# Performance work log

Hardware: AMD Instinct MI355X
Metric: run time of the kernel (lower is better)

## Reference

```python
import jax, jax.numpy as jnp
import numpy as np

B, T_ENC, T_DEC = 16, 256, 64
N_MEL = 80
ENC_DIM = 512
ATTN_RNN_DIM = 1024
DEC_RNN_DIM = 1024
PRENET_DIM = 256
ATTN_DIM = 128
LOC_FILTERS = 32
LOC_KERNEL = 31


def setup_inputs() -> dict:
    key = jax.random.key(0)
    ks = jax.random.split(key, 32)
    s = 0.02
    inp = {
        "memory": jax.random.normal(ks[0], (B, T_ENC, ENC_DIM), jnp.float32),
        "decoder_inputs": jax.random.normal(ks[1], (B, N_MEL, T_DEC), jnp.float32),
        "memory_lengths": jax.random.randint(ks[2], (B,), T_ENC // 2, T_ENC + 1, jnp.int32),
        # prenet
        "prenet_W1": jax.random.normal(ks[3], (PRENET_DIM, N_MEL), jnp.float32) * s,
        "prenet_b1": jnp.zeros((PRENET_DIM,), jnp.float32),
        "prenet_W2": jax.random.normal(ks[4], (PRENET_DIM, PRENET_DIM), jnp.float32) * s,
        "prenet_b2": jnp.zeros((PRENET_DIM,), jnp.float32),
        # attention LSTMCell: input = prenet_dim + enc_dim
        "attn_rnn_Wih": jax.random.normal(ks[5], (4 * ATTN_RNN_DIM, PRENET_DIM + ENC_DIM), jnp.float32) * s,
        "attn_rnn_Whh": jax.random.normal(ks[6], (4 * ATTN_RNN_DIM, ATTN_RNN_DIM), jnp.float32) * s,
        "attn_rnn_bih": jnp.zeros((4 * ATTN_RNN_DIM,), jnp.float32),
        "attn_rnn_bhh": jnp.zeros((4 * ATTN_RNN_DIM,), jnp.float32),
        # attention projections (bias-free, Tacotron2 style)
        "query_W": jax.random.normal(ks[7], (ATTN_DIM, ATTN_RNN_DIM), jnp.float32) * s,
        "mem_W": jax.random.normal(ks[8], (ATTN_DIM, ENC_DIM), jnp.float32) * s,
        "loc_conv_W": jax.random.normal(ks[9], (LOC_FILTERS, 2, LOC_KERNEL), jnp.float32) * s,
        "loc_dense_W": jax.random.normal(ks[10], (ATTN_DIM, LOC_FILTERS), jnp.float32) * s,
        "attn_v": jax.random.normal(ks[11], (1, ATTN_DIM), jnp.float32) * s,
        # decoder LSTMCell: input = attn_rnn_dim + enc_dim
        "dec_rnn_Wih": jax.random.normal(ks[12], (4 * DEC_RNN_DIM, ATTN_RNN_DIM + ENC_DIM), jnp.float32) * s,
        "dec_rnn_Whh": jax.random.normal(ks[13], (4 * DEC_RNN_DIM, DEC_RNN_DIM), jnp.float32) * s,
        "dec_rnn_bih": jnp.zeros((4 * DEC_RNN_DIM,), jnp.float32),
        "dec_rnn_bhh": jnp.zeros((4 * DEC_RNN_DIM,), jnp.float32),
        # output heads
        "proj_W": jax.random.normal(ks[14], (N_MEL, DEC_RNN_DIM + ENC_DIM), jnp.float32) * s,
        "proj_b": jnp.zeros((N_MEL,), jnp.float32),
        "gate_W": jax.random.normal(ks[15], (1, DEC_RNN_DIM + ENC_DIM), jnp.float32) * s,
        "gate_b": jnp.zeros((1,), jnp.float32),
    }
    return inp


def _lstm_cell(x, h, c, Wih, Whh, bih, bhh):
    gates = x @ Wih.T + bih + h @ Whh.T + bhh  # [B, 4H]
    i, f, g, o = jnp.split(gates, 4, axis=-1)
    c2 = jax.nn.sigmoid(f) * c + jax.nn.sigmoid(i) * jnp.tanh(g)
    h2 = jax.nn.sigmoid(o) * jnp.tanh(c2)
    return h2, c2


def _decoder_forward(memory, decoder_inputs, memory_lengths,
                     prenet_W1, prenet_b1, prenet_W2, prenet_b2,
                     attn_rnn_Wih, attn_rnn_Whh, attn_rnn_bih, attn_rnn_bhh,
                     query_W, mem_W, loc_conv_W, loc_dense_W, attn_v,
                     dec_rnn_Wih, dec_rnn_Whh, dec_rnn_bih, dec_rnn_bhh,
                     proj_W, proj_b, gate_W, gate_b):
    b, t_enc, _ = memory.shape
    t_dec = decoder_inputs.shape[2]
    # parse_decoder_inputs: [B,80,T] -> [T,B,80]; prepend go frame
    frames = jnp.transpose(decoder_inputs, (2, 0, 1))  # [T,B,80]
    go = jnp.zeros((1, b, N_MEL), frames.dtype)
    frames = jnp.concatenate([go, frames], axis=0)  # [T+1,B,80]
    # prenet (dropout disabled for determinism)
    pre = jax.nn.relu(frames @ prenet_W1.T + prenet_b1)
    pre = jax.nn.relu(pre @ prenet_W2.T + prenet_b2)  # [T+1,B,256]
    pre = pre[:-1]  # steps use frames 0..T-1

    processed_memory = memory @ mem_W.T  # [B,T_enc,128]
    pad_mask = jnp.arange(t_enc)[None, :] >= memory_lengths[:, None]  # [B,T_enc] True=pad

    pad = (LOC_KERNEL - 1) // 2

    def step(carry, x_t):
        (ah, ac, dh, dc, aw, aw_cum, ctx) = carry
        cell_in = jnp.concatenate([x_t, ctx], axis=-1)
        ah, ac = _lstm_cell(cell_in, ah, ac, attn_rnn_Wih, attn_rnn_Whh, attn_rnn_bih, attn_rnn_bhh)
        # location-sensitive attention
        awc = jnp.stack([aw, aw_cum], axis=1)  # [B,2,T_enc]
        loc = jax.lax.conv_general_dilated(
            awc, loc_conv_W, window_strides=(1,), padding=[(pad, pad)],
            dimension_numbers=("NCH", "OIH", "NCH"))  # [B,32,T_enc]
        loc = jnp.transpose(loc, (0, 2, 1)) @ loc_dense_W.T  # [B,T_enc,128]
        query = (ah @ query_W.T)[:, None, :]  # [B,1,128]
        energies = jnp.squeeze(jnp.tanh(query + processed_memory + loc) @ attn_v.T, -1)  # [B,T_enc]
        energies = jnp.where(pad_mask, -1e9, energies)
        aw = jax.nn.softmax(energies, axis=1)
        ctx = jnp.einsum("bt,btd->bd", aw, memory)
        aw_cum = aw_cum + aw
        dec_in = jnp.concatenate([ah, ctx], axis=-1)
        dh, dc = _lstm_cell(dec_in, dh, dc, dec_rnn_Wih, dec_rnn_Whh, dec_rnn_bih, dec_rnn_bhh)
        dhc = jnp.concatenate([dh, ctx], axis=-1)
        mel = dhc @ proj_W.T + proj_b  # [B,80]
        gate = jnp.squeeze(dhc @ gate_W.T + gate_b, -1)  # [B]
        return (ah, ac, dh, dc, aw, aw_cum, ctx), (mel, gate, aw)

    z = jnp.zeros
    carry0 = (z((b, ATTN_RNN_DIM)), z((b, ATTN_RNN_DIM)),
              z((b, DEC_RNN_DIM)), z((b, DEC_RNN_DIM)),
              z((b, t_enc)), z((b, t_enc)), z((b, ENC_DIM)))
    _, (mels, gates, aligns) = jax.lax.scan(step, carry0, pre)
    # parse_decoder_outputs
    mel_outputs = jnp.transpose(mels, (1, 2, 0))  # [B,80,T_dec]
    gate_outputs = jnp.transpose(gates, (1, 0))  # [B,T_dec]
    alignments = jnp.transpose(aligns, (1, 0, 2))  # [B,T_dec,T_enc]
    return mel_outputs, gate_outputs, alignments


def reference(memory, decoder_inputs, memory_lengths,
              prenet_W1, prenet_b1, prenet_W2, prenet_b2,
              attn_rnn_Wih, attn_rnn_Whh, attn_rnn_bih, attn_rnn_bhh,
              query_W, mem_W, loc_conv_W, loc_dense_W, attn_v,
              dec_rnn_Wih, dec_rnn_Whh, dec_rnn_bih, dec_rnn_bhh,
              proj_W, proj_b, gate_W, gate_b):
    return _decoder_forward(memory, decoder_inputs, memory_lengths,
                            prenet_W1, prenet_b1, prenet_W2, prenet_b2,
                            attn_rnn_Wih, attn_rnn_Whh, attn_rnn_bih, attn_rnn_bhh,
                            query_W, mem_W, loc_conv_W, loc_dense_W, attn_v,
                            dec_rnn_Wih, dec_rnn_Whh, dec_rnn_bih, dec_rnn_bhh,
                            proj_W, proj_b, gate_W, gate_b)
```

## Files before the change

kernel.cpp:

```cpp
#include <hip/hip_runtime.h>

typedef __attribute__((ext_vector_type(8))) short short8;
typedef __attribute__((ext_vector_type(4))) float f32x4;
typedef unsigned short u16;
typedef unsigned int u32;
typedef unsigned long long u64;


static constexpr size_t OFF_WFA   = 0;
static constexpr size_t OFF_WFD   = 14680064;
static constexpr size_t OFF_PREF  = 35651584;
static constexpr size_t OFF_QWF   = 36175872;
static constexpr size_t OFF_MWT   = 36438016;
static constexpr size_t OFF_BA    = 36700160;
static constexpr size_t OFF_BD    = 36716544;
static constexpr size_t OFF_PM    = 36732928;
static constexpr size_t OFF_CTXF  = 38830080;
static constexpr size_t OFF_DHF   = 40960000;
static constexpr size_t OFF_AHFD  = 45219840;
static constexpr size_t OFF_CTXFD = 47349760;
static constexpr size_t OFF_DHFD  = 48414720;
static constexpr size_t OFF_BAR   = 50544640;
static constexpr size_t OFF_END   = 50548736;

__device__ __forceinline__ float sigmf(float x) { return 1.f / (1.f + expf(-x)); }
__device__ __forceinline__ float tanh_fast(float x) {
  float e2 = __expf(2.f * x);
  return 1.f - 2.f / (e2 + 1.f);
}
__device__ __forceinline__ u16 f2bf(float f) {
  u32 u = __float_as_uint(f);
  return (u16)((u + 0x7FFFu + ((u >> 16) & 1u)) >> 16);
}
__device__ __forceinline__ float bf2f(u16 x) { return __uint_as_float(((u32)x) << 16); }

__device__ __forceinline__ short8 ld_frag_nt(const void* p) {
  const u64* q = (const u64*)p;
  u64 lo = __builtin_nontemporal_load(q);
  u64 hi = __builtin_nontemporal_load(q + 1);
  union { u64 q2[2]; short8 s; } u;
  u.q2[0] = lo; u.q2[1] = hi;
  return u.s;
}

__device__ __forceinline__ void st_u16_agent(u16* p, u16 v) {
  __hip_atomic_store(p, v, __ATOMIC_RELAXED, __HIP_MEMORY_SCOPE_AGENT);
}
__device__ __forceinline__ void st_f32_agent(float* p, float v) {
  __hip_atomic_store(p, v, __ATOMIC_RELAXED, __HIP_MEMORY_SCOPE_AGENT);
}
__device__ __forceinline__ void st_u64_agent(u64* p, u64 v) {
  __hip_atomic_store(p, v, __ATOMIC_RELAXED, __HIP_MEMORY_SCOPE_AGENT);
}
__device__ __forceinline__ u32 ld_u32_agent(const u32* p) {
  return __hip_atomic_load(p, __ATOMIC_RELAXED, __HIP_MEMORY_SCOPE_AGENT);
}
__device__ __forceinline__ void st_u32_agent(u32* p, u32 v) {
  __hip_atomic_store(p, v, __ATOMIC_RELAXED, __HIP_MEMORY_SCOPE_AGENT);
}

template <int SLP>
__device__ __forceinline__ void wait_one(const u32* f, u32 target, int th) {
  if (th == 0) {
    while (ld_u32_agent(f) < target) __builtin_amdgcn_s_sleep(SLP);
  }
  __syncthreads();
}

__global__ void k_wfrag(const float* __restrict__ Wih, const float* __restrict__ Whh,
                        char* __restrict__ dst, int NT, int Kih) {
  int idx = blockIdx.x * 256 + threadIdx.x;
  int l = idx & 63;
  int st = idx >> 6;
  int s = st % NT, tile = st / NT;
  int r = l & 15, kg = l >> 4;
  int j = (r >> 2) * 1024 + tile * 4 + (r & 3);
  int k0 = s * 32 + kg * 8;
  const float* src = (k0 < Kih) ? (Wih + (size_t)j * Kih + k0)
                                : (Whh + (size_t)j * 1024 + (k0 - Kih));
  short8 v;
#pragma unroll
  for (int e = 0; e < 8; ++e) v[e] = (short)f2bf(src[e]);
  *(short8*)(dst + (size_t)idx * 16) = v;
}

__global__ void k_qwfrag(const float* __restrict__ qW, char* __restrict__ dst) {
  int idx = blockIdx.x * 256 + threadIdx.x;
  int l = idx & 63, tile = idx >> 6;
  int dt = tile >> 5, kt = tile & 31;
  int j = dt * 16 + (l & 15);
  int k0 = kt * 32 + (l >> 4) * 8;
  short8 v;
#pragma unroll
  for (int e = 0; e < 8; ++e) v[e] = (short)f2bf(qW[j * 1024 + k0 + e]);
  *(short8*)(dst + (size_t)idx * 16) = v;
}

__global__ void k_smallprep(const float* __restrict__ memW,
                            const float* __restrict__ abih, const float* __restrict__ abhh,
                            const float* __restrict__ dbih, const float* __restrict__ dbhh,
                            char* __restrict__ wsb) {
  int idx = blockIdx.x * 256 + threadIdx.x;
  if (idx < 65536) {
    int k = idx >> 7, d = idx & 127;
    ((float*)(wsb + OFF_MWT))[idx] = memW[d * 512 + k];
  } else if (idx < 69632) {
    int j = idx - 65536;
    ((float*)(wsb + OFF_BA))[j] = abih[j] + abhh[j];
  } else if (idx < 73728) {
    int j = idx - 69632;
    ((float*)(wsb + OFF_BD))[j] = dbih[j] + dbhh[j];
  }
}

__global__ void k_prenet(const float* __restrict__ dec_in,
                         const float* __restrict__ W1, const float* __restrict__ b1,
                         const float* __restrict__ W2, const float* __restrict__ b2,
                         char* __restrict__ wsb) {
  int s = blockIdx.x, b = blockIdx.y, th = threadIdx.x;
  __shared__ float frame[80];
  __shared__ float h1[256];
  if (th < 80) frame[th] = (s == 0) ? 0.f : dec_in[(b * 80 + th) * 64 + (s - 1)];
  __syncthreads();
  float a = b1[th];
  const float* w1r = W1 + th * 80;
  for (int m = 0; m < 80; ++m) a += w1r[m] * frame[m];
  h1[th] = fmaxf(a, 0.f);
  __syncthreads();
  float a2 = b2[th];
  const float* w2r = W2 + th * 256;
  for (int i = 0; i < 256; ++i) a2 += w2r[i] * h1[i];
  float pre = fmaxf(a2, 0.f);
  int k = th;
  ((u16*)(wsb + OFF_PREF))[(((size_t)s * 8 + (k >> 5)) * 64 + ((k >> 3) & 3) * 16 + b) * 8 + (k & 7)] = f2bf(pre);
}

__global__ void k_pm(const float* __restrict__ memory, char* __restrict__ wsb) {
  int bk = blockIdx.x, th = threadIdx.x;
  int b = bk >> 4, t0 = (bk & 15) * 16;
  __shared__ float mrow[16 * 512];
  for (int i = 0; i < 8; ++i) {
    int fi4 = i * 256 + th;
    int tl = fi4 >> 7, k4 = (fi4 & 127) << 2;
    *(float4*)&mrow[tl * 512 + k4] =
        *(const float4*)&memory[((size_t)(b * 256 + t0 + tl)) * 512 + k4];
  }
  __syncthreads();
  int d = th & 127, tl0 = th >> 7;
  float acc[8] = {};
  const float* mWT = (const float*)(wsb + OFF_MWT);
  float* pmw = (float*)(wsb + OFF_PM);
  for (int k = 0; k < 512; ++k) {
    float w = mWT[k * 128 + d];
#pragma unroll
    for (int i = 0; i < 8; ++i) acc[i] += w * mrow[(tl0 + i * 2) * 512 + k];
  }
  for (int i = 0; i < 8; ++i)
    pmw[((size_t)(b * 256 + t0 + tl0 + i * 2)) * 128 + d] = acc[i];
}

struct KParams {
  const float* memory;
  const int* mlen;
  const float* convW;
  const float* ldW;
  const float* attnv;
  const float* projW;
  const float* projb;
  const float* gateW;
  const float* gateb;
  char* wsb;
  float* out;
};

__device__ __forceinline__ f32x4 attn_early(char* wsb, int t, int kc, int l,
                                            const short8* afE) {
  f32x4 acc = {0.f, 0.f, 0.f, 0.f};
#pragma unroll
  for (int i = 0; i < 10; ++i) {
    int pe = kc * 10 + i;
    const char* src = (pe < 8)
        ? wsb + OFF_PREF + (((size_t)t * 8 + pe) * 64 + l) * 16
        : wsb + OFF_AHFD + (((size_t)t * 32 + (pe - 8)) * 64 + l) * 16;
    short8 bv = ld_frag_nt(src);
    acc = __builtin_amdgcn_mfma_f32_16x16x32_bf16(afE[i], bv, acc, 0, 0, 0);
  }
  return acc;
}

__device__ __forceinline__ void run_dec(char* wsb, int t, int tb, int th, int l, int w,
                                        int rt, int kc, float biasD_r, float& cD,
                                        float* smC) {
  const char* wfd = wsb + OFF_WFD;
  int tIdx = tb * 2 + rt;
  f32x4 acc = {0.f, 0.f, 0.f, 0.f};
#pragma unroll
  for (int i = 0; i < 20; ++i) {
    int kt = kc * 20 + i;
    short8 av = *(const short8*)(wfd + (((size_t)tIdx * 80 + kt) * 64 + l) * 16);
    const char* src;
    if (kt < 32)      src = wsb + OFF_AHFD + (((size_t)t * 32 + kt) * 64 + l) * 16;
    else if (kt < 48) src = wsb + OFF_CTXFD + (((size_t)t * 16 + (kt - 32)) * 64 + l) * 16;
    else              src = wsb + OFF_DHFD + (((size_t)(t - 1) * 32 + (kt - 48)) * 64 + l) * 16;
    short8 bv = ld_frag_nt(src);
    acc = __builtin_amdgcn_mfma_f32_16x16x32_bf16(av, bv, acc, 0, 0, 0);
  }
#pragma unroll
  for (int r4 = 0; r4 < 4; ++r4)
    smC[w * 256 + ((l >> 4) * 4 + r4) * 16 + (l & 15)] = acc[r4];
  __syncthreads();
  {
    int rt2 = th >> 8, r = (th >> 4) & 15, b2 = th & 15;
    float s = 0.f;
#pragma unroll
    for (int q = 0; q < 4; ++q) s += smC[(q * 2 + rt2) * 256 + r * 16 + b2];
    smC[4096 + th] = s + biasD_r;
  }
  __syncthreads();
  if (th < 128) {
    int b = th & 15, lu = th >> 4;
    int rt3 = lu >> 2, ul = lu & 3;
    int u = (tb * 2 + rt3) * 4 + ul;
    float gi = smC[4096 + rt3 * 256 + ul * 16 + b];
    float gf = smC[4096 + rt3 * 256 + (4 + ul) * 16 + b];
    float gc = smC[4096 + rt3 * 256 + (8 + ul) * 16 + b];
    float go = smC[4096 + rt3 * 256 + (12 + ul) * 16 + b];
    float c2 = sigmf(gf) * cD + sigmf(gi) * tanhf(gc);
    float h2 = sigmf(go) * tanhf(c2);
    cD = c2;
    st_f32_agent((float*)(wsb + OFF_DHF) + ((size_t)t * 1024 + u) * 16 + b, h2);
    st_u16_agent((u16*)(wsb + OFF_DHFD) +
                 ((((size_t)t * 32 + (u >> 5)) * 64 + ((u >> 3) & 3) * 16 + b) * 8 + (u & 7)),
                 f2bf(h2));
  }
}

__global__ void __launch_bounds__(512, 1) k_main(KParams p) {
  const int th = threadIdx.x;
  const int bk = blockIdx.x;
  char* wsb = p.wsb;
  const int l = th & 63, w = th >> 6;
  u32* Af = (u32*)(wsb + OFF_BAR);
  u32* Df = (u32*)(wsb + OFF_BAR + 1024);
  u32* Bf = (u32*)(wsb + OFF_BAR + 2048);
  u32* Aall = (u32*)(wsb + OFF_BAR + 3072);
  u32* Dall = (u32*)(wsb + OFF_BAR + 3136);
  u32* Ball = (u32*)(wsb + OFF_BAR + 3200);

  __shared__ float smC[4608];
  __shared__ float s2q[128], s2v[128];
  __shared__ u16 s_convF[8192];
  __shared__ u16 s_pack[512];
  __shared__ float s_e[256], s3wr[4];
  __shared__ float s1cw[1984];
  __shared__ float s_aw[256], s_awc[256];

  const float* pm = (const float*)(wsb + OFF_PM);

  if (bk < 16) {
    for (int i = th; i < 1984; i += 512) s1cw[i] = p.convW[i];
    for (int i = th; i < 4096; i += 512) ((u32*)s_convF)[i] = 0u;
    if (th < 128) s2v[th] = p.attnv[th];
    if (th < 256) { s_aw[th] = 0.f; s_awc[th] = 0.f; }
  }

  float biasA_r = 0.f, biasD_r = 0.f;
  if (bk >= 16 && bk < 144) {
    int r = (th >> 4) & 15, rt2 = th >> 8, tbase = (bk - 16) * 2;
    biasA_r = ((const float*)(wsb + OFF_BA))[(r >> 2) * 1024 + (tbase + rt2) * 4 + (r & 3)];
    biasD_r = ((const float*)(wsb + OFF_BD))[(r >> 2) * 1024 + (tbase + rt2) * 4 + (r & 3)];
  }
  int lenB = 0;
  if (bk < 16) lenB = p.mlen[bk];
  float cA = 0.f, cD = 0.f;

  const int rt = w & 1, kc = w >> 1;
  short8 afE[10], afL[4];
  if (bk >= 16 && bk < 144) {
    const char* wfa = wsb + OFF_WFA;
    int tIdx = (bk - 16) * 2 + rt;
#pragma unroll
    for (int i = 0; i < 10; ++i) {
      int pe = kc * 10 + i;
      int kt = (pe < 8) ? pe : (24 + (pe - 8));
      afE[i] = *(const short8*)(wfa + (((size_t)tIdx * 56 + kt) * 64 + l) * 16);
    }
#pragma unroll
    for (int i = 0; i < 4; ++i) {
      int kt = 8 + kc * 4 + i;
      afL[i] = *(const short8*)(wfa + (((size_t)tIdx * 56 + kt) * 64 + l) * 16);
    }
  }
  short8 ldwB[8];
  if (bk < 16) {
    int kg = l >> 4, dcol = l & 15;
#pragma unroll
    for (int dt = 0; dt < 8; ++dt) {
      short8 v;
#pragma unroll
      for (int e = 0; e < 8; ++e)
        v[e] = (short)f2bf(p.ldW[(dt * 16 + dcol) * 32 + kg * 8 + e]);
      ldwB[dt] = v;
    }
  }
  __syncthreads();

  if (bk >= 16 && bk < 144) {
    const int tb = bk - 16;
    f32x4 acc = attn_early(wsb, 0, kc, l, afE);
    for (int t = 0; t < 64; ++t) {
      wait_one<1>(Ball, (u32)t, th);
#pragma unroll
      for (int i = 0; i < 4; ++i) {
        int ct = kc * 4 + i;
        short8 bv = ld_frag_nt(wsb + OFF_CTXFD + (((size_t)t * 16 + ct) * 64 + l) * 16);
        acc = __builtin_amdgcn_mfma_f32_16x16x32_bf16(afL[i], bv, acc, 0, 0, 0);
      }
#pragma unroll
      for (int r4 = 0; r4 < 4; ++r4)
        smC[w * 256 + ((l >> 4) * 4 + r4) * 16 + (l & 15)] = acc[r4];
      __syncthreads();
      {
        int rt2 = th >> 8, r = (th >> 4) & 15, b2 = th & 15;
        float s = 0.f;
#pragma unroll
        for (int q = 0; q < 4; ++q) s += smC[(q * 2 + rt2) * 256 + r * 16 + b2];
        smC[4096 + th] = s + biasA_r;
      }
      __syncthreads();
      if (th < 128) {
        int b = th & 15, lu = th >> 4;
        float gi = smC[4096 + (lu >> 2) * 256 + (lu & 3) * 16 + b];
        float gf = smC[4096 + (lu >> 2) * 256 + (4 + (lu & 3)) * 16 + b];
        float gc = smC[4096 + (lu >> 2) * 256 + (8 + (lu & 3)) * 16 + b];
        float go = smC[4096 + (lu >> 2) * 256 + (12 + (lu & 3)) * 16 + b];
        float c2 = sigmf(gf) * cA + sigmf(gi) * tanhf(gc);
        float h2 = sigmf(go) * tanhf(c2);
        cA = c2;
        s_pack[b * 8 + lu] = f2bf(h2);
      }
      __syncthreads();
      if (th < 16) {
        const u64* src = (const u64*)s_pack + th * 2;
        u64* dst = (u64*)(wsb + OFF_AHFD + ((size_t)(t + 1) * 32 + (tb >> 2)) * 1024 +
                          ((size_t)(tb & 3) * 16 + th) * 16);
        st_u64_agent(dst, src[0]);
        st_u64_agent(dst + 1, src[1]);
      }
      __syncthreads();
      if (th == 0) st_u32_agent(Af + tb, (u32)(t + 1));
      if (t >= 1) {
        wait_one<1>(Dall, (u32)(t - 1), th);
        run_dec(wsb, t, tb, th, l, w, rt, kc, biasD_r, cD, smC);
        __syncthreads();
        if (th == 0) st_u32_agent(Df + tb, (u32)t);
      }
      if (t < 63) {
        wait_one<1>(Aall, (u32)(t + 1), th);
        acc = attn_early(wsb, t + 1, kc, l, afE);
      }
    }
    wait_one<1>(Ball, 64u, th);
    wait_one<1>(Dall, 63u, th);
    run_dec(wsb, 64, tb, th, l, w, rt, kc, biasD_r, cD, smC);
    __syncthreads();
    if (th == 0) st_u32_agent(Df + tb, 64u);
  } else if (bk < 16) {
    const int b = bk;
    for (int t = 0; t < 64; ++t) {
      {
        int jmax = (lenB + 15) >> 4;
        for (int j = 0; j < jmax; ++j) {
          int idx = j * 512 + th, tt = idx >> 5, f = idx & 31;
          float a = 0.f;
          const float* w0 = s1cw + f * 62;
#pragma unroll
          for (int kk = 0; kk < 31; ++kk) {
            int pos = tt + kk - 15;
            bool ok = (pos >= 0 && pos < 256);
            float awv = ok ? s_aw[pos] : 0.f;
            float awcv = ok ? s_awc[pos] : 0.f;
            a += awv * w0[kk] + awcv * w0[31 + kk];
          }
          s_convF[(tt >> 4) * 512 + ((f >> 3) * 16 + (tt & 15)) * 8 + (f & 7)] = f2bf(a);
        }
      }
      wait_one<1>(Aall, (u32)(t + 1), th);
      {
        f32x4 qacc = {0.f, 0.f, 0.f, 0.f};
        const char* qwf = wsb + OFF_QWF;
#pragma unroll 4
        for (int kt = 0; kt < 32; ++kt) {
          short8 av = *(const short8*)(qwf + (((size_t)w * 32 + kt) * 64 + l) * 16);
          short8 bv = ld_frag_nt(wsb + OFF_AHFD + ((size_t)(t + 1) * 32 + kt) * 1024 +
                                 ((size_t)(l >> 4) * 16 + b) * 16);
          qacc = __builtin_amdgcn_mfma_f32_16x16x32_bf16(av, bv, qacc, 0, 0, 0);
        }
        if ((l & 15) == 0) {
          int r0 = (l >> 4) * 4;
          s2q[w * 16 + r0]     = qacc[0];
          s2q[w * 16 + r0 + 1] = qacc[1];
          s2q[w * 16 + r0 + 2] = qacc[2];
          s2q[w * 16 + r0 + 3] = qacc[3];
        }
      }
      __syncthreads();
      {
#pragma unroll
        for (int tl = 0; tl < 2; ++tl) {
          int ttile = w * 2 + tl;
          short8 afc = *(const short8*)&s_convF[ttile * 512 + l * 8];
          int dcol = l & 15;
          float e0 = 0.f, e1 = 0.f, e2 = 0.f, e3 = 0.f;
          const float* pmb = pm + ((size_t)(b * 256 + ttile * 16 + (l >> 4) * 4)) * 128 + dcol;
#pragma unroll
          for (int dt = 0; dt < 8; ++dt) {
            f32x4 S = {0.f, 0.f, 0.f, 0.f};
            S = __builtin_amdgcn_mfma_f32_16x16x32_bf16(afc, ldwB[dt], S, 0, 0, 0);
            int d = dt * 16 + dcol;
            float qd = s2q[d], vd = s2v[d];
            e0 += vd * tanh_fast(qd + pmb[dt * 16 + 0 * 128] + S[0]);
            e1 += vd * tanh_fast(qd + pmb[dt * 16 + 1 * 128] + S[1]);
            e2 += vd * tanh_fast(qd + pmb[dt * 16 + 2 * 128] + S[2]);
            e3 += vd * tanh_fast(qd + pmb[dt * 16 + 3 * 128] + S[3]);
          }
#pragma unroll
          for (int off = 8; off; off >>= 1) {
            e0 += __shfl_xor(e0, off);
            e1 += __shfl_xor(e1, off);
            e2 += __shfl_xor(e2, off);
            e3 += __shfl_xor(e3, off);
          }
          if ((l & 15) == 0) {
            int tb0 = ttile * 16 + (l >> 4) * 4;
            s_e[tb0]     = (tb0     < lenB) ? __expf(e0) : 0.f;
            s_e[tb0 + 1] = (tb0 + 1 < lenB) ? __expf(e1) : 0.f;
            s_e[tb0 + 2] = (tb0 + 2 < lenB) ? __expf(e2) : 0.f;
            s_e[tb0 + 3] = (tb0 + 3 < lenB) ? __expf(e3) : 0.f;
          }
        }
      }
      __syncthreads();
      if (th < 256) {
        float v0 = s_e[th];
#pragma unroll
        for (int off = 32; off; off >>= 1) v0 += __shfl_xor(v0, off);
        if ((th & 63) == 0) s3wr[th >> 6] = v0;
      }
      __syncthreads();
      float rden = 1.f / (s3wr[0] + s3wr[1] + s3wr[2] + s3wr[3]);
      if (th < 256) {
        float a = s_e[th] * rden;
        s_aw[th] = a;
        s_awc[th] += a;
        p.out[82944 + ((size_t)(b * 64 + t)) * 256 + th] = a;
      }
      __syncthreads();
      {
        int dq = th & 127, tg = th >> 7;
        int d0 = dq * 4;
        float a0 = 0.f, a1 = 0.f, a2 = 0.f, a3 = 0.f;
        const float* mb = p.memory + ((size_t)b * 256) * 512 + d0;
        for (int tt = tg; tt < lenB; tt += 4) {
          float4 mv = *(const float4*)(mb + (size_t)tt * 512);
          float aw = s_aw[tt];
          a0 += aw * mv.x; a1 += aw * mv.y; a2 += aw * mv.z; a3 += aw * mv.w;
        }
        smC[tg * 512 + d0]     = a0;
        smC[tg * 512 + d0 + 1] = a1;
        smC[tg * 512 + d0 + 2] = a2;
        smC[tg * 512 + d0 + 3] = a3;
      }
      __syncthreads();
      {
        int d = th;
        float ctxv = smC[d] + smC[512 + d] + smC[1024 + d] + smC[1536 + d];
        st_f32_agent((float*)(wsb + OFF_CTXF) + (size_t)(t + 1) * 8192 + b * 512 + d, ctxv);
        s_pack[d] = f2bf(ctxv);
      }
      __syncthreads();
      if (th < 64) {
        u64 p0 = ((const u64*)s_pack)[th * 2];
        u64 p1 = ((const u64*)s_pack)[th * 2 + 1];
        u64* dst = (u64*)(wsb + OFF_CTXFD + ((size_t)(t + 1) * 16 + (th >> 2)) * 1024 +
                          ((size_t)(th & 3) * 16 + b) * 16);
        st_u64_agent(dst, p0);
        st_u64_agent(dst + 1, p1);
      }
      __syncthreads();
      if (th == 0) st_u32_agent(Bf + b * 16, (u32)(t + 1));
    }
  } else if (bk == 144) {
    if (th < 64) {
      for (u32 tgt = 1; tgt <= 64; ++tgt) {
        for (;;) {
          u32 v0 = ld_u32_agent(Af + th);
          u32 v1 = ld_u32_agent(Af + 64 + th);
          u32 mn = v0 < v1 ? v0 : v1;
          if (__all(mn >= tgt)) break;
          __builtin_amdgcn_s_sleep(1);
        }
        if (th == 0) st_u32_agent(Aall, tgt);
      }
    }
    __syncthreads();
  } else if (bk == 145) {
    if (th < 64) {
      for (u32 tgt = 1; tgt <= 64; ++tgt) {
        for (;;) {
          u32 v0 = ld_u32_agent(Df + th);
          u32 v1 = ld_u32_agent(Df + 64 + th);
          u32 mn = v0 < v1 ? v0 : v1;
          if (__all(mn >= tgt)) break;
          __builtin_amdgcn_s_sleep(1);
        }
        if (th == 0) st_u32_agent(Dall, tgt);
      }
    }
    __syncthreads();
  } else if (bk == 146) {
    if (th < 64) {
      for (u32 tgt = 1; tgt <= 64; ++tgt) {
        for (;;) {
          u32 v = ld_u32_agent(Bf + (th & 15) * 16);
          if (__all(v >= tgt)) break;
          __builtin_amdgcn_s_sleep(1);
        }
        if (th == 0) st_u32_agent(Ball, tgt);
      }
    }
    __syncthreads();
  }

  if (bk >= 147) {
    wait_one<64>(Dall, 64u, th);
    wait_one<64>(Ball, 64u, th);
  } else {
    wait_one<4>(Dall, 64u, th);
    wait_one<4>(Ball, 64u, th);
  }
  {
    int t = bk & 63, pa = bk >> 6;
    const float* dh = (const float*)(wsb + OFF_DHF) + (size_t)(t + 1) * 16384;
    const float* cxt = (const float*)(wsb + OFF_CTXF) + (size_t)(t + 1) * 8192;
    int lim = (pa == 3) ? 336 : 320;
    for (int idx = th; idx < lim; idx += 512) {
      if (idx < 320) {
        int mi = idx >> 4, b = idx & 15, m = pa * 20 + mi;
        const float* wr = p.projW + (size_t)m * 1536;
        const float* cxb = cxt + b * 512;
        float a0 = 0.f, a1 = 0.f;
#pragma unroll 8
        for (int k = 0; k < 1024; k += 2) { a0 += wr[k] * dh[k * 16 + b]; a1 += wr[k + 1] * dh[(k + 1) * 16 + b]; }
#pragma unroll 8
        for (int k = 0; k < 512; k += 2)  { a0 += wr[1024 + k] * cxb[k]; a1 += wr[1025 + k] * cxb[k + 1]; }
        p.out[((size_t)(b * 80 + m)) * 64 + t] = a0 + a1 + p.projb[m];
      } else {
        int b = idx - 320;
        const float* cxb = cxt + b * 512;
        float a0 = 0.f, a1 = 0.f;
#pragma unroll 8
        for (int k = 0; k < 1024; k += 2) { a0 += p.gateW[k] * dh[k * 16 + b]; a1 += p.gateW[k + 1] * dh[(k + 1) * 16 + b]; }
#pragma unroll 8
        for (int k = 0; k < 512; k += 2)  { a0 += p.gateW[1024 + k] * cxb[k]; a1 += p.gateW[1025 + k] * cxb[k + 1]; }
        p.out[81920 + b * 64 + t] = a0 + a1 + p.gateb[0];
      }
    }
  }
}

extern "C" void kernel_launch(void* const* d_in, const int* in_sizes, int n_in,
                              void* d_out, int out_size, void* d_ws, size_t ws_size,
                              hipStream_t stream) {
  (void)in_sizes; (void)n_in; (void)out_size; (void)ws_size;
  const float* memory = (const float*)d_in[0];
  const float* dec_in = (const float*)d_in[1];
  const int*   mlen   = (const int*)d_in[2];
  const float* pW1    = (const float*)d_in[3];
  const float* pb1    = (const float*)d_in[4];
  const float* pW2    = (const float*)d_in[5];
  const float* pb2    = (const float*)d_in[6];
  const float* aWih   = (const float*)d_in[7];
  const float* aWhh   = (const float*)d_in[8];
  const float* abih   = (const float*)d_in[9];
  const float* abhh   = (const float*)d_in[10];
  const float* qW     = (const float*)d_in[11];
  const float* memW   = (const float*)d_in[12];
  const float* convW  = (const float*)d_in[13];
  const float* ldW    = (const float*)d_in[14];
  const float* attnv  = (const float*)d_in[15];
  const float* dWih   = (const float*)d_in[16];
  const float* dWhh   = (const float*)d_in[17];
  const float* dbih   = (const float*)d_in[18];
  const float* dbhh   = (const float*)d_in[19];
  const float* projW  = (const float*)d_in[20];
  const float* projb  = (const float*)d_in[21];
  const float* gateW  = (const float*)d_in[22];
  const float* gateb  = (const float*)d_in[23];
  char* wsb = (char*)d_ws;
  float* out = (float*)d_out;

  hipMemsetAsync(wsb + OFF_AHFD, 0, 32768, stream);
  hipMemsetAsync(wsb + OFF_CTXFD, 0, 16384, stream);
  hipMemsetAsync(wsb + OFF_DHFD, 0, 32768, stream);
  hipMemsetAsync(wsb + OFF_BAR, 0, 4096, stream);

  hipLaunchKernelGGL(k_wfrag, dim3(3584), dim3(256), 0, stream, aWih, aWhh, wsb + OFF_WFA, 56, 768);
  hipLaunchKernelGGL(k_wfrag, dim3(5120), dim3(256), 0, stream, dWih, dWhh, wsb + OFF_WFD, 80, 1536);
  hipLaunchKernelGGL(k_qwfrag, dim3(64), dim3(256), 0, stream, qW, wsb + OFF_QWF);
  hipLaunchKernelGGL(k_smallprep, dim3(288), dim3(256), 0, stream, memW, abih, abhh, dbih, dbhh, wsb);
  hipLaunchKernelGGL(k_prenet, dim3(64, 16), dim3(256), 0, stream, dec_in, pW1, pb1, pW2, pb2, wsb);
  hipLaunchKernelGGL(k_pm, dim3(256), dim3(256), 0, stream, memory, wsb);

  KParams p{memory, mlen, convW, ldW, attnv, projW, projb, gateW, gateb, wsb, out};
  void* args[] = { &p };
  hipLaunchCooperativeKernel((void*)k_main, dim3(256), dim3(512), args, 0, stream);
}
```

Before: 2.783 ms.

## Split LSTM cells onto dedicated 16-block groups with direct flag polling

Replaces the 128 combined attention/decoder LSTM blocks with 16 blocks for the attention LSTM and 16 separate blocks for the decoder LSTM. Each warp now computes two gate tiles and does its own LSTM pointwise update, so one cross-warp reduction is removed. The aggregator blocks that collapsed per-block flags into single 'all' counters are gone; waiters poll the 16 producer flags directly with a wave vote. Weight fragments now stream from global memory each step instead of sitting in registers. Running the decoder on its own blocks lets it overlap with the attention pipeline, at the cost of fewer blocks and more weight traffic per block.

```diff
diff --git a/kernel.cpp b/kernel.cpp
--- a/kernel.cpp
+++ b/kernel.cpp
@@ -34,6 +34,9 @@
 }
 __device__ __forceinline__ float bf2f(u16 x) { return __uint_as_float(((u32)x) << 16); }
 
+__device__ __forceinline__ short8 ld_frag(const void* p) {
+  return *(const short8*)p;
+}
 __device__ __forceinline__ short8 ld_frag_nt(const void* p) {
   const u64* q = (const u64*)p;
   u64 lo = __builtin_nontemporal_load(q);
@@ -60,9 +63,14 @@
 }
 
 template <int SLP>
-__device__ __forceinline__ void wait_one(const u32* f, u32 target, int th) {
-  if (th == 0) {
-    while (ld_u32_agent(f) < target) __builtin_amdgcn_s_sleep(SLP);
+__device__ __forceinline__ void wait16(const u32* F, u32 target, int th) {
+  if (th < 64) {
+    const u32* pf = F + (th & 15) * 16;
+    for (;;) {
+      u32 v = ld_u32_agent(pf);
+      if (__all(v >= target)) break;
+      __builtin_amdgcn_s_sleep(SLP);
+    }
   }
   __syncthreads();
 }
@@ -173,68 +181,6 @@
   float* out;
 };
 
-__device__ __forceinline__ f32x4 attn_early(char* wsb, int t, int kc, int l,
-                                            const short8* afE) {
-  f32x4 acc = {0.f, 0.f, 0.f, 0.f};
-#pragma unroll
-  for (int i = 0; i < 10; ++i) {
-    int pe = kc * 10 + i;
-    const char* src = (pe < 8)
-        ? wsb + OFF_PREF + (((size_t)t * 8 + pe) * 64 + l) * 16
-        : wsb + OFF_AHFD + (((size_t)t * 32 + (pe - 8)) * 64 + l) * 16;
-    short8 bv = ld_frag_nt(src);
-    acc = __builtin_amdgcn_mfma_f32_16x16x32_bf16(afE[i], bv, acc, 0, 0, 0);
-  }
-  return acc;
-}
-
-__device__ __forceinline__ void run_dec(char* wsb, int t, int tb, int th, int l, int w,
-                                        int rt, int kc, float biasD_r, float& cD,
-                                        float* smC) {
-  const char* wfd = wsb + OFF_WFD;
-  int tIdx = tb * 2 + rt;
-  f32x4 acc = {0.f, 0.f, 0.f, 0.f};
-#pragma unroll
-  for (int i = 0; i < 20; ++i) {
-    int kt = kc * 20 + i;
-    short8 av = *(const short8*)(wfd + (((size_t)tIdx * 80 + kt) * 64 + l) * 16);
-    const char* src;
-    if (kt < 32)      src = wsb + OFF_AHFD + (((size_t)t * 32 + kt) * 64 + l) * 16;
-    else if (kt < 48) src = wsb + OFF_CTXFD + (((size_t)t * 16 + (kt - 32)) * 64 + l) * 16;
-    else              src = wsb + OFF_DHFD + (((size_t)(t - 1) * 32 + (kt - 48)) * 64 + l) * 16;
-    short8 bv = ld_frag_nt(src);
-    acc = __builtin_amdgcn_mfma_f32_16x16x32_bf16(av, bv, acc, 0, 0, 0);
-  }
-#pragma unroll
-  for (int r4 = 0; r4 < 4; ++r4)
-    smC[w * 256 + ((l >> 4) * 4 + r4) * 16 + (l & 15)] = acc[r4];
-  __syncthreads();
-  {
-    int rt2 = th >> 8, r = (th >> 4) & 15, b2 = th & 15;
-    float s = 0.f;
-#pragma unroll
-    for (int q = 0; q < 4; ++q) s += smC[(q * 2 + rt2) * 256 + r * 16 + b2];
-    smC[4096 + th] = s + biasD_r;
-  }
-  __syncthreads();
-  if (th < 128) {
-    int b = th & 15, lu = th >> 4;
-    int rt3 = lu >> 2, ul = lu & 3;
-    int u = (tb * 2 + rt3) * 4 + ul;
-    float gi = smC[4096 + rt3 * 256 + ul * 16 + b];
-    float gf = smC[4096 + rt3 * 256 + (4 + ul) * 16 + b];
-    float gc = smC[4096 + rt3 * 256 + (8 + ul) * 16 + b];
-    float go = smC[4096 + rt3 * 256 + (12 + ul) * 16 + b];
-    float c2 = sigmf(gf) * cD + sigmf(gi) * tanhf(gc);
-    float h2 = sigmf(go) * tanhf(c2);
-    cD = c2;
-    st_f32_agent((float*)(wsb + OFF_DHF) + ((size_t)t * 1024 + u) * 16 + b, h2);
-    st_u16_agent((u16*)(wsb + OFF_DHFD) +
-                 ((((size_t)t * 32 + (u >> 5)) * 64 + ((u >> 3) & 3) * 16 + b) * 8 + (u & 7)),
-                 f2bf(h2));
-  }
-}
-
 __global__ void __launch_bounds__(512, 1) k_main(KParams p) {
   const int th = threadIdx.x;
   const int bk = blockIdx.x;
@@ -243,9 +189,6 @@
   u32* Af = (u32*)(wsb + OFF_BAR);
   u32* Df = (u32*)(wsb + OFF_BAR + 1024);
   u32* Bf = (u32*)(wsb + OFF_BAR + 2048);
-  u32* Aall = (u32*)(wsb + OFF_BAR + 3072);
-  u32* Dall = (u32*)(wsb + OFF_BAR + 3136);
-  u32* Ball = (u32*)(wsb + OFF_BAR + 3200);
 
   __shared__ float smC[4608];
   __shared__ float s2q[128], s2v[128];
@@ -254,6 +197,8 @@
   __shared__ float s_e[256], s3wr[4];
   __shared__ float s1cw[1984];
   __shared__ float s_aw[256], s_awc[256];
+  __shared__ float smW[4096];
+  __shared__ u16 sp[1024];
 
   const float* pm = (const float*)(wsb + OFF_PM);
 
@@ -263,34 +208,9 @@
     if (th < 128) s2v[th] = p.attnv[th];
     if (th < 256) { s_aw[th] = 0.f; s_awc[th] = 0.f; }
   }
-
-  float biasA_r = 0.f, biasD_r = 0.f;
-  if (bk >= 16 && bk < 144) {
-    int r = (th >> 4) & 15, rt2 = th >> 8, tbase = (bk - 16) * 2;
-    biasA_r = ((const float*)(wsb + OFF_BA))[(r >> 2) * 1024 + (tbase + rt2) * 4 + (r & 3)];
-    biasD_r = ((const float*)(wsb + OFF_BD))[(r >> 2) * 1024 + (tbase + rt2) * 4 + (r & 3)];
-  }
   int lenB = 0;
   if (bk < 16) lenB = p.mlen[bk];
-  float cA = 0.f, cD = 0.f;
-
-  const int rt = w & 1, kc = w >> 1;
-  short8 afE[10], afL[4];
-  if (bk >= 16 && bk < 144) {
-    const char* wfa = wsb + OFF_WFA;
-    int tIdx = (bk - 16) * 2 + rt;
-#pragma unroll
-    for (int i = 0; i < 10; ++i) {
-      int pe = kc * 10 + i;
-      int kt = (pe < 8) ? pe : (24 + (pe - 8));
-      afE[i] = *(const short8*)(wfa + (((size_t)tIdx * 56 + kt) * 64 + l) * 16);
-    }
-#pragma unroll
-    for (int i = 0; i < 4; ++i) {
-      int kt = 8 + kc * 4 + i;
-      afL[i] = *(const short8*)(wfa + (((size_t)tIdx * 56 + kt) * 64 + l) * 16);
-    }
-  }
+
   short8 ldwB[8];
   if (bk < 16) {
     int kg = l >> 4, dcol = l & 15;
@@ -305,73 +225,169 @@
   }
   __syncthreads();
 
-  if (bk >= 16 && bk < 144) {
-    const int tb = bk - 16;
-    f32x4 acc = attn_early(wsb, 0, kc, l, afE);
+  if (bk >= 16 && bk < 32) {
+    const int i = bk - 16;
+    const char* wfa = wsb + OFF_WFA;
+    const int tI0 = i * 16 + w * 2;
+    float bA[2][4], cA2[2] = {0.f, 0.f};
+    {
+      const float* ba = (const float*)(wsb + OFF_BA);
+#pragma unroll
+      for (int pq = 0; pq < 2; ++pq) {
+        int idx = l * 2 + pq, lu = idx >> 4;
+        int u = i * 64 + w * 8 + lu;
+#pragma unroll
+        for (int g = 0; g < 4; ++g) bA[pq][g] = ba[g * 1024 + u];
+      }
+    }
+    f32x4 acc0, acc1;
+    auto EARLY = [&](int t) {
+      acc0 = f32x4{0.f, 0.f, 0.f, 0.f};
+      acc1 = f32x4{0.f, 0.f, 0.f, 0.f};
+      for (int e = 0; e < 40; ++e) {
+        int s = (e < 8) ? e : (24 + (e - 8));
+        const char* bsrc = (e < 8)
+            ? wsb + OFF_PREF + (((size_t)t * 8 + s) * 64 + l) * 16
+            : wsb + OFF_AHFD + (((size_t)t * 32 + (s - 24)) * 64 + l) * 16;
+        short8 bv = ld_frag(bsrc);
+        short8 a0 = *(const short8*)(wfa + (((size_t)tI0 * 56 + s) * 64 + l) * 16);
+        short8 a1 = *(const short8*)(wfa + (((size_t)(tI0 + 1) * 56 + s) * 64 + l) * 16);
+        acc0 = __builtin_amdgcn_mfma_f32_16x16x32_bf16(a0, bv, acc0, 0, 0, 0);
+        acc1 = __builtin_amdgcn_mfma_f32_16x16x32_bf16(a1, bv, acc1, 0, 0, 0);
+      }
+    };
+    EARLY(0);
     for (int t = 0; t < 64; ++t) {
-      wait_one<1>(Ball, (u32)t, th);
-#pragma unroll
-      for (int i = 0; i < 4; ++i) {
-        int ct = kc * 4 + i;
-        short8 bv = ld_frag_nt(wsb + OFF_CTXFD + (((size_t)t * 16 + ct) * 64 + l) * 16);
-        acc = __builtin_amdgcn_mfma_f32_16x16x32_bf16(afL[i], bv, acc, 0, 0, 0);
-      }
-#pragma unroll
-      for (int r4 = 0; r4 < 4; ++r4)
-        smC[w * 256 + ((l >> 4) * 4 + r4) * 16 + (l & 15)] = acc[r4];
-      __syncthreads();
-      {
-        int rt2 = th >> 8, r = (th >> 4) & 15, b2 = th & 15;
-        float s = 0.f;
-#pragma unroll
-        for (int q = 0; q < 4; ++q) s += smC[(q * 2 + rt2) * 256 + r * 16 + b2];
-        smC[4096 + th] = s + biasA_r;
-      }
-      __syncthreads();
-      if (th < 128) {
-        int b = th & 15, lu = th >> 4;
-        float gi = smC[4096 + (lu >> 2) * 256 + (lu & 3) * 16 + b];
-        float gf = smC[4096 + (lu >> 2) * 256 + (4 + (lu & 3)) * 16 + b];
-        float gc = smC[4096 + (lu >> 2) * 256 + (8 + (lu & 3)) * 16 + b];
-        float go = smC[4096 + (lu >> 2) * 256 + (12 + (lu & 3)) * 16 + b];
-        float c2 = sigmf(gf) * cA + sigmf(gi) * tanhf(gc);
-        float h2 = sigmf(go) * tanhf(c2);
-        cA = c2;
-        s_pack[b * 8 + lu] = f2bf(h2);
-      }
-      __syncthreads();
-      if (th < 16) {
-        const u64* src = (const u64*)s_pack + th * 2;
-        u64* dst = (u64*)(wsb + OFF_AHFD + ((size_t)(t + 1) * 32 + (tb >> 2)) * 1024 +
-                          ((size_t)(tb & 3) * 16 + th) * 16);
+      wait16<1>(Bf, (u32)t, th);
+#pragma unroll
+      for (int s = 8; s < 24; ++s) {
+        short8 bv = ld_frag(wsb + OFF_CTXFD + (((size_t)t * 16 + (s - 8)) * 64 + l) * 16);
+        short8 a0 = *(const short8*)(wfa + (((size_t)tI0 * 56 + s) * 64 + l) * 16);
+        short8 a1 = *(const short8*)(wfa + (((size_t)(tI0 + 1) * 56 + s) * 64 + l) * 16);
+        acc0 = __builtin_amdgcn_mfma_f32_16x16x32_bf16(a0, bv, acc0, 0, 0, 0);
+        acc1 = __builtin_amdgcn_mfma_f32_16x16x32_bf16(a1, bv, acc1, 0, 0, 0);
+      }
+      {
+        float* myW = smW + w * 512;
+#pragma unroll
+        for (int r4 = 0; r4 < 4; ++r4) {
+          myW[((l >> 4) * 4 + r4) * 16 + (l & 15)] = acc0[r4];
+          myW[256 + ((l >> 4) * 4 + r4) * 16 + (l & 15)] = acc1[r4];
+        }
+      }
+      __syncthreads();
+      {
+        const float* myW = smW + w * 512;
+        u16* myP = sp + w * 128;
+#pragma unroll
+        for (int pq = 0; pq < 2; ++pq) {
+          int idx = l * 2 + pq, lu = idx >> 4, b = idx & 15;
+          int rt = lu >> 2, uoff = lu & 3;
+          float gi = myW[rt * 256 + (0 * 4 + uoff) * 16 + b] + bA[pq][0];
+          float gf = myW[rt * 256 + (1 * 4 + uoff) * 16 + b] + bA[pq][1];
+          float gg = myW[rt * 256 + (2 * 4 + uoff) * 16 + b] + bA[pq][2];
+          float go = myW[rt * 256 + (3 * 4 + uoff) * 16 + b] + bA[pq][3];
+          float c2 = sigmf(gf) * cA2[pq] + sigmf(gi) * tanhf(gg);
+          float h2 = sigmf(go) * tanhf(c2);
+          cA2[pq] = c2;
+          myP[b * 8 + lu] = f2bf(h2);
+        }
+      }
+      __syncthreads();
+      if (l < 16) {
+        const u64* src = (const u64*)(sp + w * 128) + l * 2;
+        int slab = i * 8 + w;
+        u64* dst = (u64*)(wsb + OFF_AHFD + ((size_t)(t + 1) * 32 + (slab >> 2)) * 1024 +
+                          ((size_t)((slab & 3) * 16 + l)) * 16);
         st_u64_agent(dst, src[0]);
         st_u64_agent(dst + 1, src[1]);
       }
       __syncthreads();
-      if (th == 0) st_u32_agent(Af + tb, (u32)(t + 1));
-      if (t >= 1) {
-        wait_one<1>(Dall, (u32)(t - 1), th);
-        run_dec(wsb, t, tb, th, l, w, rt, kc, biasD_r, cD, smC);
-        __syncthreads();
-        if (th == 0) st_u32_agent(Df + tb, (u32)t);
-      }
+      if (th == 0) st_u32_agent(Af + i * 16, (u32)(t + 1));
       if (t < 63) {
-        wait_one<1>(Aall, (u32)(t + 1), th);
-        acc = attn_early(wsb, t + 1, kc, l, afE);
-      }
-    }
-    wait_one<1>(Ball, 64u, th);
-    wait_one<1>(Dall, 63u, th);
-    run_dec(wsb, 64, tb, th, l, w, rt, kc, biasD_r, cD, smC);
-    __syncthreads();
-    if (th == 0) st_u32_agent(Df + tb, 64u);
+        wait16<1>(Af, (u32)(t + 1), th);
+        EARLY(t + 1);
+      }
+    }
+  } else if (bk >= 32 && bk < 48) {
+    const int j = bk - 32;
+    const char* wfd = wsb + OFF_WFD;
+    const int tI0 = j * 16 + w * 2;
+    float bD[2][4], cD2[2] = {0.f, 0.f};
+    {
+      const float* bd = (const float*)(wsb + OFF_BD);
+#pragma unroll
+      for (int pq = 0; pq < 2; ++pq) {
+        int idx = l * 2 + pq, lu = idx >> 4;
+        int u = j * 64 + w * 8 + lu;
+#pragma unroll
+        for (int g = 0; g < 4; ++g) bD[pq][g] = bd[g * 1024 + u];
+      }
+    }
+    for (int t = 1; t <= 64; ++t) {
+      wait16<2>(Af, (u32)t, th);
+      wait16<2>(Bf, (u32)t, th);
+      if (t >= 2) wait16<2>(Df, (u32)(t - 1), th);
+      f32x4 acc0 = {0.f, 0.f, 0.f, 0.f}, acc1 = {0.f, 0.f, 0.f, 0.f};
+      for (int s = 0; s < 80; ++s) {
+        const char* bsrc;
+        if (s < 32)      bsrc = wsb + OFF_AHFD + (((size_t)t * 32 + s) * 64 + l) * 16;
+        else if (s < 48) bsrc = wsb + OFF_CTXFD + (((size_t)t * 16 + (s - 32)) * 64 + l) * 16;
+        else             bsrc = wsb + OFF_DHFD + (((size_t)(t - 1) * 32 + (s - 48)) * 64 + l) * 16;
+        short8 bv = ld_frag_nt(bsrc);
+        short8 a0 = ld_frag_nt(wfd + (((size_t)tI0 * 80 + s) * 64 + l) * 16);
+        short8 a1 = ld_frag_nt(wfd + (((size_t)(tI0 + 1) * 80 + s) * 64 + l) * 16);
+        acc0 = __builtin_amdgcn_mfma_f32_16x16x32_bf16(a0, bv, acc0, 0, 0, 0);
+        acc1 = __builtin_amdgcn_mfma_f32_16x16x32_bf16(a1, bv, acc1, 0, 0, 0);
+      }
+      {
+        float* myW = smW + w * 512;
+#pragma unroll
+        for (int r4 = 0; r4 < 4; ++r4) {
+          myW[((l >> 4) * 4 + r4) * 16 + (l & 15)] = acc0[r4];
+          myW[256 + ((l >> 4) * 4 + r4) * 16 + (l & 15)] = acc1[r4];
+        }
+      }
+      __syncthreads();
+      {
+        const float* myW = smW + w * 512;
+        u16* myP = sp + w * 128;
+        float* dhf = (float*)(wsb + OFF_DHF);
+#pragma unroll
+        for (int pq = 0; pq < 2; ++pq) {
+          int idx = l * 2 + pq, lu = idx >> 4, b = idx & 15;
+          int rt = lu >> 2, uoff = lu & 3;
+          float gi = myW[rt * 256 + (0 * 4 + uoff) * 16 + b] + bD[pq][0];
+          float gf = myW[rt * 256 + (1 * 4 + uoff) * 16 + b] + bD[pq][1];
+          float gg = myW[rt * 256 + (2 * 4 + uoff) * 16 + b] + bD[pq][2];
+          float go = myW[rt * 256 + (3 * 4 + uoff) * 16 + b] + bD[pq][3];
+          float c2 = sigmf(gf) * cD2[pq] + sigmf(gi) * tanhf(gg);
+          float h2 = sigmf(go) * tanhf(c2);
+          cD2[pq] = c2;
+          int u = j * 64 + w * 8 + lu;
+          st_f32_agent(dhf + ((size_t)t * 1024 + u) * 16 + b, h2);
+          myP[b * 8 + lu] = f2bf(h2);
+        }
+      }
+      __syncthreads();
+      if (l < 16) {
+        const u64* src = (const u64*)(sp + w * 128) + l * 2;
+        int slab = j * 8 + w;
+        u64* dst = (u64*)(wsb + OFF_DHFD + ((size_t)t * 32 + (slab >> 2)) * 1024 +
+                          ((size_t)((slab & 3) * 16 + l)) * 16);
+        st_u64_agent(dst, src[0]);
+        st_u64_agent(dst + 1, src[1]);
+      }
+      __syncthreads();
+      if (th == 0) st_u32_agent(Df + j * 16, (u32)t);
+    }
   } else if (bk < 16) {
     const int b = bk;
     for (int t = 0; t < 64; ++t) {
       {
         int jmax = (lenB + 15) >> 4;
-        for (int j = 0; j < jmax; ++j) {
-          int idx = j * 512 + th, tt = idx >> 5, f = idx & 31;
+        for (int jj = 0; jj < jmax; ++jj) {
+          int idx = jj * 512 + th, tt = idx >> 5, f = idx & 31;
           float a = 0.f;
           const float* w0 = s1cw + f * 62;
 #pragma unroll
@@ -385,15 +401,15 @@
           s_convF[(tt >> 4) * 512 + ((f >> 3) * 16 + (tt & 15)) * 8 + (f & 7)] = f2bf(a);
         }
       }
-      wait_one<1>(Aall, (u32)(t + 1), th);
+      wait16<1>(Af, (u32)(t + 1), th);
       {
         f32x4 qacc = {0.f, 0.f, 0.f, 0.f};
         const char* qwf = wsb + OFF_QWF;
 #pragma unroll 4
         for (int kt = 0; kt < 32; ++kt) {
           short8 av = *(const short8*)(qwf + (((size_t)w * 32 + kt) * 64 + l) * 16);
-          short8 bv = ld_frag_nt(wsb + OFF_AHFD + ((size_t)(t + 1) * 32 + kt) * 1024 +
-                                 ((size_t)(l >> 4) * 16 + b) * 16);
+          short8 bv = ld_frag(wsb + OFF_AHFD + ((size_t)(t + 1) * 32 + kt) * 1024 +
+                              ((size_t)(l >> 4) * 16 + b) * 16);
           qacc = __builtin_amdgcn_mfma_f32_16x16x32_bf16(av, bv, qacc, 0, 0, 0);
         }
         if ((l & 15) == 0) {
@@ -490,54 +506,14 @@
       __syncthreads();
       if (th == 0) st_u32_agent(Bf + b * 16, (u32)(t + 1));
     }
-  } else if (bk == 144) {
-    if (th < 64) {
-      for (u32 tgt = 1; tgt <= 64; ++tgt) {
-        for (;;) {
-          u32 v0 = ld_u32_agent(Af + th);
-          u32 v1 = ld_u32_agent(Af + 64 + th);
-          u32 mn = v0 < v1 ? v0 : v1;
-          if (__all(mn >= tgt)) break;
-          __builtin_amdgcn_s_sleep(1);
-        }
-        if (th == 0) st_u32_agent(Aall, tgt);
-      }
-    }
-    __syncthreads();
-  } else if (bk == 145) {
-    if (th < 64) {
-      for (u32 tgt = 1; tgt <= 64; ++tgt) {
-        for (;;) {
-          u32 v0 = ld_u32_agent(Df + th);
-          u32 v1 = ld_u32_agent(Df + 64 + th);
-          u32 mn = v0 < v1 ? v0 : v1;
-          if (__all(mn >= tgt)) break;
-          __builtin_amdgcn_s_sleep(1);
-        }
-        if (th == 0) st_u32_agent(Dall, tgt);
-      }
-    }
-    __syncthreads();
-  } else if (bk == 146) {
-    if (th < 64) {
-      for (u32 tgt = 1; tgt <= 64; ++tgt) {
-        for (;;) {
-          u32 v = ld_u32_agent(Bf + (th & 15) * 16);
-          if (__all(v >= tgt)) break;
-          __builtin_amdgcn_s_sleep(1);
-        }
-        if (th == 0) st_u32_agent(Ball, tgt);
-      }
-    }
-    __syncthreads();
-  }
-
-  if (bk >= 147) {
-    wait_one<64>(Dall, 64u, th);
-    wait_one<64>(Ball, 64u, th);
+  }
+
+  if (bk >= 48) {
+    wait16<64>(Df, 64u, th);
+    wait16<64>(Bf, 64u, th);
   } else {
-    wait_one<4>(Dall, 64u, th);
-    wait_one<4>(Ball, 64u, th);
+    wait16<4>(Df, 64u, th);
+    wait16<4>(Bf, 64u, th);
   }
   {
     int t = bk & 63, pa = bk >> 6;
```

Result: slower. 3.180 ms (+14.3%).
